# Performance work log

Measured on AMD Instinct MI355X. Metric: run time of the kernel, lower is better.

## Reference

```python
import jax, jax.numpy as jnp
import numpy as np

FACE_W = 256   # cube face width W; output equirect is (2W, 4W)
CH = 32        # channels
BATCH = 2
EPS = 1e-9


def _equi_grid(in_w):
    """Reproduces _config(): per output pixel, the source cube face id and the
    normalized [-1,1] sampling coords on that face (align_corners=True convention).
    Faces: 0:+x 1:-x 2:+y 3:-y 4:+z 5:-z."""
    out_h, out_w = 2 * in_w, 4 * in_w
    yy, xx = jnp.meshgrid(jnp.arange(out_h, dtype=jnp.float32),
                          jnp.arange(out_w, dtype=jnp.float32), indexing='ij')
    theta = (2.0 * (xx + 0.5) / out_w - 1.0) * jnp.pi           # longitude in [-pi, pi)
    phi = (2.0 * (yy + 0.5) / out_h - 1.0) * (jnp.pi / 2.0)     # latitude  in [-pi/2, pi/2)
    # xy2angle + to_3dsphere(theta, phi, R=1)
    x = jnp.cos(phi) * jnp.cos(theta)
    y = jnp.cos(phi) * jnp.sin(theta)
    z = jnp.sin(phi)
    ax, ay, az = jnp.abs(x), jnp.abs(y), jnp.abs(z)
    # get_face: dominant axis decides the cube face
    face = jnp.where((ax >= ay) & (ax >= az), jnp.where(x >= 0, 0, 1),
           jnp.where(ay >= az,                jnp.where(y >= 0, 2, 3),
                                              jnp.where(z >= 0, 4, 5)))
    axs = jnp.maximum(ax, EPS)
    ays = jnp.maximum(ay, EPS)
    azs = jnp.maximum(az, EPS)
    # face_to_cube_coord: project ray onto the face plane -> (u, v) in [-1, 1]
    u = jnp.select([face == 0, face == 1, face == 2, face == 3, face == 4, face == 5],
                   [y / axs, -y / axs, -x / ays, x / ays, y / azs, y / azs])
    v = jnp.select([face <= 1, face <= 3, face == 4, face == 5],
                   [z / axs, z / ays, -x / azs, x / azs])
    # norm_to_cube maps to [0, W-1]; forward then renormalizes via
    # (g - max/2)/(max/2) back to [-1, 1] -> (u, v) directly, align_corners=True.
    return face, u, v


def _cube2equi(input_data):
    # input_data: (B, 6, C, W, W) -> (B, C, 2W, 4W)
    B, F, C, W, _ = input_data.shape
    face, u, v = _equi_grid(W)                      # (out_h, out_w) each
    # align_corners=True: [-1,1] -> [0, W-1]
    px = (u + 1.0) * 0.5 * (W - 1)
    py = (v + 1.0) * 0.5 * (W - 1)
    x0 = jnp.floor(px)
    y0 = jnp.floor(py)
    wx = (px - x0)[..., None]                       # (out_h, out_w, 1)
    wy = (py - y0)[..., None]
    x0i = jnp.clip(x0, 0, W - 1).astype(jnp.int32)
    x1i = jnp.clip(x0 + 1, 0, W - 1).astype(jnp.int32)
    y0i = jnp.clip(y0, 0, W - 1).astype(jnp.int32)
    y1i = jnp.clip(y0 + 1, 0, W - 1).astype(jnp.int32)

    def sample_one(img):                            # img: (6, C, W, W)
        g = lambda yi, xi: img[face, :, yi, xi]     # fused per-pixel face pick + gather -> (out_h, out_w, C)
        out = (g(y0i, x0i) * (1.0 - wx) * (1.0 - wy)
               + g(y0i, x1i) * wx * (1.0 - wy)
               + g(y1i, x0i) * (1.0 - wx) * wy
               + g(y1i, x1i) * wx * wy)
        return jnp.transpose(out, (2, 0, 1))        # (C, out_h, out_w)

    return jax.vmap(sample_one)(input_data)


def setup_inputs() -> dict:
    key = jax.random.key(0)
    input_data = jax.random.normal(key, (BATCH, 6, CH, FACE_W, FACE_W), dtype=jnp.float32)
    return {"input_data": input_data}


def reference(input_data) -> jnp.ndarray:
    return _cube2equi(input_data)
```

## Files before the change

### kernel.cpp

```cpp
#include <hip/hip_runtime.h>
#include <hip/hip_fp16.h>
#include <math.h>

#define FACE_W 256
#define CH 32
#define BATCH 2
#define OUT_H (2 * FACE_W)
#define OUT_W (4 * FACE_W)
#define N_PIX (OUT_H * OUT_W)
#define PLANE (FACE_W * FACE_W)
#define FACE_STRIDE (CH * PLANE)
#define BATCH_STRIDE (6 * FACE_STRIDE)
#define OUT_PLANE (OUT_H * OUT_W)

#define TRANS_H_ELEMS ((size_t)BATCH * 6 * PLANE * CH)
#define TRANS_H_BYTES (TRANS_H_ELEMS * 2)
#define REC_BYTES     ((size_t)N_PIX * 8)

#define TPOSE_BLOCKS (BATCH * 6 * (PLANE / 64))
#define GRID_BLOCKS  (N_PIX / 256)

__device__ __forceinline__ float2 h2f2(unsigned u) {
    union { unsigned u; __half2 h; } c;
    c.u = u;
    return __half22float2(c.h);
}

__global__ __launch_bounds__(256) void prep_kernel(
    const float* __restrict__ in, ushort* __restrict__ out_h,
    uint2* __restrict__ rec) {
    if (blockIdx.x < TPOSE_BLOCKS) {
        __shared__ ushort tile[64][CH + 2];
        int bf  = blockIdx.x >> 10;
        int p0  = (blockIdx.x & 1023) << 6;
        int tid = threadIdx.x;

        const float* src = in + (size_t)bf * FACE_STRIDE + p0;
        int pl = tid & 63, c0 = tid >> 6;
        #pragma unroll
        for (int c = c0; c < CH; c += 4)
            tile[pl][c] = __half_as_ushort(__float2half(src[(size_t)c * PLANE + pl]));
        __syncthreads();

        unsigned* dst = (unsigned*)(out_h + ((size_t)bf * PLANE + p0) * CH);
        int cl = tid & 15, pl2 = tid >> 4;
        #pragma unroll
        for (int k = 0; k < 4; ++k) {
            int p = pl2 + 16 * k;
            dst[p * (CH / 2) + cl] = *(const unsigned*)&tile[p][2 * cl];
        }
    } else {
        int pix = (blockIdx.x - TPOSE_BLOCKS) * 256 + threadIdx.x;
        int xx = pix & (OUT_W - 1);
        int yy = pix >> 10;

        const double PI = 3.14159265358979323846;
        double theta = (2.0 * (xx + 0.5) / OUT_W - 1.0) * PI;
        double phi   = (2.0 * (yy + 0.5) / OUT_H - 1.0) * (PI * 0.5);
        double cph = cos(phi);
        double sx = cph * cos(theta);
        double sy = cph * sin(theta);
        double sz = sin(phi);
        double ax = fabs(sx), ay = fabs(sy), az = fabs(sz);

        const double EPS = 1e-9;
        int face;
        double u, v;
        if (ax >= ay && ax >= az) {
            face = (sx >= 0.0) ? 0 : 1;
            double d = fmax(ax, EPS);
            u = ((face == 0) ? sy : -sy) / d;
            v = sz / d;
        } else if (ay >= az) {
            face = (sy >= 0.0) ? 2 : 3;
            double d = fmax(ay, EPS);
            u = ((face == 2) ? -sx : sx) / d;
            v = sz / d;
        } else {
            face = (sz >= 0.0) ? 4 : 5;
            double d = fmax(az, EPS);
            u = sy / d;
            v = ((face == 4) ? -sx : sx) / d;
        }

        float px = (float)((u + 1.0) * 0.5 * (FACE_W - 1));
        float py = (float)((v + 1.0) * 0.5 * (FACE_W - 1));
        float fx0 = floorf(px), fy0 = floorf(py);
        float wx = px - fx0, wy = py - fy0;
        int x0 = min(max((int)fx0, 0), FACE_W - 1);
        int y0 = min(max((int)fy0, 0), FACE_W - 1);

        unsigned off00 = ((unsigned)face << 16) | (unsigned)(y0 * FACE_W + x0);
        unsigned wpack = (unsigned)__half_as_ushort(__float2half(wx)) |
                         ((unsigned)__half_as_ushort(__float2half(wy)) << 16);
        rec[pix] = make_uint2(off00, wpack);
    }
}

__global__ __launch_bounds__(256) void sample_h_kernel(
    const ushort* __restrict__ in_h, const uint2* __restrict__ rec,
    float* __restrict__ out) {
    unsigned g = blockIdx.x * blockDim.x + threadIdx.x;
    int cg  = g & 3;
    int pix = g >> 2;

    uint2 r = rec[pix];
    int face  = r.x >> 16;
    int pix16 = r.x & 0xFFFF;
    int x0 = r.x & 255;
    int y0 = (r.x >> 8) & 255;
    float wx = __half2float(__ushort_as_half((ushort)(r.y & 0xFFFF)));
    float wy = __half2float(__ushort_as_half((ushort)(r.y >> 16)));
    int dxE = (x0 < FACE_W - 1) ? CH : 0;
    int dyE = (y0 < FACE_W - 1) ? FACE_W * CH : 0;

    float w00 = (1.0f - wx) * (1.0f - wy);
    float w10 = wx * (1.0f - wy);
    float w01 = (1.0f - wx) * wy;
    float w11 = wx * wy;

    const ushort* s0 = in_h + ((size_t)face * PLANE + pix16) * CH + cg * 8;

    #pragma unroll
    for (int b = 0; b < BATCH; ++b) {
        const ushort* sb = s0 + (size_t)b * (6 * (size_t)PLANE * CH);
        uint4 q00 = *(const uint4*)(sb);
        uint4 q10 = *(const uint4*)(sb + dxE);
        uint4 q01 = *(const uint4*)(sb + dyE);
        uint4 q11 = *(const uint4*)(sb + dxE + dyE);

        float* ob = out + ((size_t)(b * CH + cg * 8)) * OUT_PLANE + pix;
        #pragma unroll
        for (int j = 0; j < 4; ++j) {
            float2 f00 = h2f2(((const unsigned*)&q00)[j]);
            float2 f10 = h2f2(((const unsigned*)&q10)[j]);
            float2 f01 = h2f2(((const unsigned*)&q01)[j]);
            float2 f11 = h2f2(((const unsigned*)&q11)[j]);
            ob[(size_t)(2 * j) * OUT_PLANE] =
                f00.x * w00 + f10.x * w10 + f01.x * w01 + f11.x * w11;
            ob[(size_t)(2 * j + 1) * OUT_PLANE] =
                f00.y * w00 + f10.y * w10 + f01.y * w01 + f11.y * w11;
        }
    }
}

__global__ __launch_bounds__(256) void cube2equi_fused(
    const float* __restrict__ in, float* __restrict__ out) {
    int pix = blockIdx.x * blockDim.x + threadIdx.x;
    if (pix >= N_PIX) return;
    int xx = pix & (OUT_W - 1);
    int yy = pix >> 10;

    const double PI = 3.14159265358979323846;
    double theta = (2.0 * (xx + 0.5) / OUT_W - 1.0) * PI;
    double phi   = (2.0 * (yy + 0.5) / OUT_H - 1.0) * (PI * 0.5);
    double cph = cos(phi);
    double sx = cph * cos(theta);
    double sy = cph * sin(theta);
    double sz = sin(phi);
    double ax = fabs(sx), ay = fabs(sy), az = fabs(sz);

    const double EPS = 1e-9;
    int face;
    double u, v;
    if (ax >= ay && ax >= az) {
        face = (sx >= 0.0) ? 0 : 1;
        double d = fmax(ax, EPS);
        u = ((face == 0) ? sy : -sy) / d;
        v = sz / d;
    } else if (ay >= az) {
        face = (sy >= 0.0) ? 2 : 3;
        double d = fmax(ay, EPS);
        u = ((face == 2) ? -sx : sx) / d;
        v = sz / d;
    } else {
        face = (sz >= 0.0) ? 4 : 5;
        double d = fmax(az, EPS);
        u = sy / d;
        v = ((face == 4) ? -sx : sx) / d;
    }

    float px = (float)((u + 1.0) * 0.5 * (FACE_W - 1));
    float py = (float)((v + 1.0) * 0.5 * (FACE_W - 1));
    float fx0 = floorf(px), fy0 = floorf(py);
    float wx = px - fx0, wy = py - fy0;
    int x0 = min(max((int)fx0, 0), FACE_W - 1);
    int x1 = min(max((int)fx0 + 1, 0), FACE_W - 1);
    int y0 = min(max((int)fy0, 0), FACE_W - 1);
    int y1 = min(max((int)fy0 + 1, 0), FACE_W - 1);

    float w00 = (1.0f - wx) * (1.0f - wy);
    float w10 = wx * (1.0f - wy);
    float w01 = (1.0f - wx) * wy;
    float w11 = wx * wy;

    int o00 = y0 * FACE_W + x0;
    int o10 = y0 * FACE_W + x1;
    int o01 = y1 * FACE_W + x0;
    int o11 = y1 * FACE_W + x1;

    const float* fbase = in + (size_t)face * FACE_STRIDE;

    for (int b = 0; b < BATCH; ++b) {
        const float* bb = fbase + (size_t)b * BATCH_STRIDE;
        float* obp = out + (size_t)b * CH * OUT_PLANE + pix;
        #pragma unroll 4
        for (int c = 0; c < CH; ++c) {
            const float* p = bb + (size_t)c * PLANE;
            obp[(size_t)c * OUT_PLANE] = p[o00] * w00 + p[o10] * w10 +
                                         p[o01] * w01 + p[o11] * w11;
        }
    }
}

extern "C" void kernel_launch(void* const* d_in, const int* in_sizes, int n_in,
                              void* d_out, int out_size, void* d_ws, size_t ws_size,
                              hipStream_t stream) {
    const float* in = (const float*)d_in[0];
    float* out = (float*)d_out;

    if (ws_size >= TRANS_H_BYTES + REC_BYTES) {
        ushort* in_h = (ushort*)d_ws;
        uint2* rec = (uint2*)((char*)d_ws + TRANS_H_BYTES);
        prep_kernel<<<TPOSE_BLOCKS + GRID_BLOCKS, 256, 0, stream>>>(in, in_h, rec);
        sample_h_kernel<<<(N_PIX * 4) / 256, 256, 0, stream>>>(in_h, rec, out);
    } else {
        cube2equi_fused<<<N_PIX / 256, 256, 0, stream>>>(in, out);
    }
}
```

Measured before the change: 242.6 us.

## Widen transpose tiles with vector nontemporal loads and remap sample block order

The transpose part of the prep kernel now handles 256 pixels per block, reading float4 vectors with nontemporal loads and writing 16-byte packed half rows per thread. The sample kernel remaps block indices so consecutive hardware blocks land in eight strided regions, and it writes outputs with nontemporal stores. The aim is wider, more coalesced memory transactions and less cache pollution from streaming data. The trade-offs are a larger LDS tile per block, which can lower occupancy, and LDS bank conflicts from the 4-pixel strided writes.

```diff
diff --git a/kernel.cpp b/kernel.cpp
--- a/kernel.cpp
+++ b/kernel.cpp
@@ -17,37 +17,62 @@
 #define TRANS_H_BYTES (TRANS_H_ELEMS * 2)
 #define REC_BYTES     ((size_t)N_PIX * 8)
 
-#define TPOSE_BLOCKS (BATCH * 6 * (PLANE / 64))
+#define TPOSE_BLOCKS (BATCH * 6 * (PLANE / 256))
 #define GRID_BLOCKS  (N_PIX / 256)
+#define SAMPLE_BLOCKS ((N_PIX * 4) / 256)
+
+typedef float  f4  __attribute__((ext_vector_type(4)));
+typedef unsigned u4v __attribute__((ext_vector_type(4)));
 
 __device__ __forceinline__ float2 h2f2(unsigned u) {
     union { unsigned u; __half2 h; } c;
     c.u = u;
     return __half22float2(c.h);
 }
+__device__ __forceinline__ unsigned packh2(float a, float b) {
+    union { __half2 h; unsigned u; } c;
+    c.h = __halves2half2(__float2half(a), __float2half(b));
+    return c.u;
+}
 
 __global__ __launch_bounds__(256) void prep_kernel(
     const float* __restrict__ in, ushort* __restrict__ out_h,
     uint2* __restrict__ rec) {
     if (blockIdx.x < TPOSE_BLOCKS) {
-        __shared__ ushort tile[64][CH + 2];
-        int bf  = blockIdx.x >> 10;
-        int p0  = (blockIdx.x & 1023) << 6;
+        __shared__ ushort tile[256][CH + 2];
+        int bf  = blockIdx.x >> 8;
+        int p0  = (blockIdx.x & 255) << 8;
         int tid = threadIdx.x;
-
-        const float* src = in + (size_t)bf * FACE_STRIDE + p0;
-        int pl = tid & 63, c0 = tid >> 6;
-        #pragma unroll
-        for (int c = c0; c < CH; c += 4)
-            tile[pl][c] = __half_as_ushort(__float2half(src[(size_t)c * PLANE + pl]));
+        int l = tid & 63, w = tid >> 6;
+
+        const float* src = in + (size_t)bf * FACE_STRIDE + p0 + 4 * l;
+        f4 A[4], B[4];
+        #pragma unroll
+        for (int it = 0; it < 4; ++it) {
+            int cp = it * 4 + w;
+            A[it] = __builtin_nontemporal_load(
+                        (const f4*)(src + (size_t)(2 * cp) * PLANE));
+            B[it] = __builtin_nontemporal_load(
+                        (const f4*)(src + (size_t)(2 * cp + 1) * PLANE));
+        }
+        #pragma unroll
+        for (int it = 0; it < 4; ++it) {
+            int cp = it * 4 + w;
+            #pragma unroll
+            for (int i = 0; i < 4; ++i)
+                *(unsigned*)&tile[4 * l + i][2 * cp] = packh2(A[it][i], B[it][i]);
+        }
         __syncthreads();
 
-        unsigned* dst = (unsigned*)(out_h + ((size_t)bf * PLANE + p0) * CH);
-        int cl = tid & 15, pl2 = tid >> 4;
-        #pragma unroll
-        for (int k = 0; k < 4; ++k) {
-            int p = pl2 + 16 * k;
-            dst[p * (CH / 2) + cl] = *(const unsigned*)&tile[p][2 * cl];
+        const ushort* row = tile[tid];
+        uint4* dst = (uint4*)(out_h + ((size_t)bf * PLANE + p0 + tid) * CH);
+        #pragma unroll
+        for (int q = 0; q < 4; ++q) {
+            unsigned u0 = *(const unsigned*)&row[8 * q + 0];
+            unsigned u1 = *(const unsigned*)&row[8 * q + 2];
+            unsigned u2 = *(const unsigned*)&row[8 * q + 4];
+            unsigned u3 = *(const unsigned*)&row[8 * q + 6];
+            dst[q] = make_uint4(u0, u1, u2, u3);
         }
     } else {
         int pix = (blockIdx.x - TPOSE_BLOCKS) * 256 + threadIdx.x;
@@ -100,7 +125,8 @@
 __global__ __launch_bounds__(256) void sample_h_kernel(
     const ushort* __restrict__ in_h, const uint2* __restrict__ rec,
     float* __restrict__ out) {
-    unsigned g = blockIdx.x * blockDim.x + threadIdx.x;
+    unsigned bid = (blockIdx.x & 7) * (SAMPLE_BLOCKS / 8) + (blockIdx.x >> 3);
+    unsigned g = bid * blockDim.x + threadIdx.x;
     int cg  = g & 3;
     int pix = g >> 2;
 
@@ -136,10 +162,12 @@
             float2 f10 = h2f2(((const unsigned*)&q10)[j]);
             float2 f01 = h2f2(((const unsigned*)&q01)[j]);
             float2 f11 = h2f2(((const unsigned*)&q11)[j]);
-            ob[(size_t)(2 * j) * OUT_PLANE] =
-                f00.x * w00 + f10.x * w10 + f01.x * w01 + f11.x * w11;
-            ob[(size_t)(2 * j + 1) * OUT_PLANE] =
-                f00.y * w00 + f10.y * w10 + f01.y * w01 + f11.y * w11;
+            __builtin_nontemporal_store(
+                f00.x * w00 + f10.x * w10 + f01.x * w01 + f11.x * w11,
+                &ob[(size_t)(2 * j) * OUT_PLANE]);
+            __builtin_nontemporal_store(
+                f00.y * w00 + f10.y * w10 + f01.y * w01 + f11.y * w11,
+                &ob[(size_t)(2 * j + 1) * OUT_PLANE]);
         }
     }
 }
@@ -223,7 +251,7 @@
         ushort* in_h = (ushort*)d_ws;
         uint2* rec = (uint2*)((char*)d_ws + TRANS_H_BYTES);
         prep_kernel<<<TPOSE_BLOCKS + GRID_BLOCKS, 256, 0, stream>>>(in, in_h, rec);
-        sample_h_kernel<<<(N_PIX * 4) / 256, 256, 0, stream>>>(in_h, rec, out);
+        sample_h_kernel<<<SAMPLE_BLOCKS, 256, 0, stream>>>(in_h, rec, out);
     } else {
         cube2equi_fused<<<N_PIX / 256, 256, 0, stream>>>(in, out);
     }
```

Measured after the change: 230.5 us. -5.0%, faster.
